# Optimization experiments

Hardware: AMD Instinct MI355X
Metric: run time of the kernel (lower is better)

The kernel has to match this reference:

```python
import jax, jax.numpy as jnp
import numpy as np

NUM_ENVS = 16384
N = 12          # decision vars (4 legs x 3D force)
M_CON = 24      # 4 SOC cones (3 each) + 12-dim hardtanh box
A_MIN, A_MAX = -10.0, 10.0
ALPHA, BETA = 1.0, 1.0


def setup_inputs() -> dict:
    key = jax.random.key(0)
    k1, k2, k3, k4 = jax.random.split(key, 4)
    Mw = jax.random.normal(k1, (NUM_ENVS, N, N), dtype=jnp.float32) / np.sqrt(N)
    # P must be SPD for inv/solve as in the original QP setup
    P = Mw @ jnp.swapaxes(Mw, -1, -2) + jnp.eye(N, dtype=jnp.float32)
    q = jax.random.normal(k2, (NUM_ENVS, N), dtype=jnp.float32)
    H = jax.random.normal(k3, (NUM_ENVS, M_CON, N), dtype=jnp.float32) * 0.5
    b = jax.random.normal(k4, (NUM_ENVS, M_CON), dtype=jnp.float32)
    contact_filter = jnp.ones((NUM_ENVS, M_CON), dtype=jnp.float32)
    return {"P": P, "q": q, "H": H, "b": b, "contact_filter": contact_filter, "iters": 100}


def _project(z, cf):
    # z: [B, m, 1]. Faithful to torch: project_onto_soc's only in-place effect on z
    # is z_part *= (z_part[:, 2:3] > 0); the full cone projection result is
    # discarded (returned but never written back). Then hardtanh box, then contact filter.
    Bsz = z.shape[0]
    soc = z[:, :12].reshape(Bsz, 4, 3)               # 4 cones of dim 3
    soc = soc * (soc[:, :, 2:3] > 0)                 # zero cone block if z-component <= 0
    box = jnp.clip(z[:, 12:24], A_MIN, A_MAX)        # hardtanh
    z = jnp.concatenate([soc.reshape(Bsz, 12, 1), box], axis=1)
    return z * cf


def reference(P, q, H, b, contact_filter, iters):
    m = H.shape[1]
    q_ = q[..., None]                                # [B, n, 1]
    b_ = b[..., None]                                # [B, m, 1]
    cf = contact_filter[..., None]                   # [B, m, 1]
    Ht = jnp.swapaxes(H, -1, -2)
    I = jnp.eye(m, dtype=P.dtype)
    Fm = I - H @ jnp.linalg.inv(P + Ht @ H) @ Ht     # [B, m, m]
    mu = Fm @ (H @ jnp.linalg.solve(P, q_) - b_)     # [B, m, 1]
    A = jnp.concatenate([
        jnp.concatenate([Fm, BETA * Fm], axis=2),
        jnp.concatenate([ALPHA * (I - 2.0 * Fm), I - 2.0 * ALPHA * BETA * Fm], axis=2),
    ], axis=1)                                       # [B, 2m, 2m]
    Bv = jnp.concatenate([BETA * mu, -2.0 * ALPHA * BETA * mu], axis=1)  # [B, 2m, 1]

    def step(lz, _):
        lz = A @ lz + Bv
        lz = jnp.concatenate([lz[:, :m], _project(lz[:, m:], cf)], axis=1)
        return lz, None

    lz0 = jnp.zeros((P.shape[0], 2 * m, 1), dtype=P.dtype)
    lz, _ = jax.lax.scan(step, lz0, None, length=iters)
    x = jnp.linalg.pinv(H) @ (lz[:, m:] - b_)        # [B, n, 1]
    return x, lz
```

## Files before the change

### kernel.cpp

```cpp
#include <hip/hip_runtime.h>

#define EPB 32
#define BLOCK 128
#define HS 292
#define GS 148
#define SS 28

#define WFENCE() __builtin_amdgcn_wave_barrier()

#define DPP_XOR1 0xB1
#define DPP_XOR2 0x4E
#define DPP_QP3  0x1B

typedef float f2 __attribute__((ext_vector_type(2)));

__device__ __forceinline__ f2 pkfma(f2 a, f2 b, f2 c) {
  return __builtin_elementwise_fma(a, b, c);
}

#define FMA4(acc, f, s)                                         \
  acc = fmaf((f).x, (s).x,                                      \
        fmaf((f).y, (s).y,                                      \
        fmaf((f).z, (s).z,                                      \
        fmaf((f).w, (s).w, (acc)))))

#define VFMA(acc, s, v)                                         \
  { (acc).x = fmaf((s), (v).x, (acc).x);                        \
    (acc).y = fmaf((s), (v).y, (acc).y);                        \
    (acc).z = fmaf((s), (v).z, (acc).z);                        \
    (acc).w = fmaf((s), (v).w, (acc).w); }

#define ADD4(A, B) { (A).x += (B).x; (A).y += (B).y; (A).z += (B).z; (A).w += (B).w; }

template<int CTRL>
__device__ __forceinline__ float dppv(float v) {
  return __int_as_float(__builtin_amdgcn_update_dpp(
      0, __float_as_int(v), CTRL, 0xF, 0xF, true));
}

template<int K>
__device__ __forceinline__ float getel(const float4& a, const float4& b, const float4& c) {
  if constexpr (K == 0) return a.x; else if constexpr (K == 1) return a.y;
  else if constexpr (K == 2) return a.z; else if constexpr (K == 3) return a.w;
  else if constexpr (K == 4) return b.x; else if constexpr (K == 5) return b.y;
  else if constexpr (K == 6) return b.z; else if constexpr (K == 7) return b.w;
  else if constexpr (K == 8) return c.x; else if constexpr (K == 9) return c.y;
  else if constexpr (K == 10) return c.z; else return c.w;
}
template<int K>
__device__ __forceinline__ void setel(float4& a, float4& b, float4& c, float v) {
  if constexpr (K == 0) a.x = v; else if constexpr (K == 1) a.y = v;
  else if constexpr (K == 2) a.z = v; else if constexpr (K == 3) a.w = v;
  else if constexpr (K == 4) b.x = v; else if constexpr (K == 5) b.y = v;
  else if constexpr (K == 6) b.z = v; else if constexpr (K == 7) b.w = v;
  else if constexpr (K == 8) c.x = v; else if constexpr (K == 9) c.y = v;
  else if constexpr (K == 10) c.z = v; else c.w = v;
}

__device__ __forceinline__ float dot12(float4 a0, float4 a1, float4 a2,
                                       const float* p) {
  const float4* p4 = (const float4*)p;
  float4 b0 = p4[0], b1 = p4[1], b2 = p4[2];
  float acc = 0.f;
  FMA4(acc, a0, b0); FMA4(acc, a1, b1); FMA4(acc, a2, b2);
  return acc;
}

template<int K>
__device__ __forceinline__ void pivot_pub(float4& a, float4& b, float4& c, float* piv) {
  float ip = 1.0f / getel<K>(a, b, c);
  setel<K>(a, b, c, 1.0f);
  a.x *= ip; a.y *= ip; a.z *= ip; a.w *= ip;
  b.x *= ip; b.y *= ip; b.z *= ip; b.w *= ip;
  c.x *= ip; c.y *= ip; c.z *= ip; c.w *= ip;
  float4* pv = (float4*)piv;
  pv[0] = a; pv[1] = b; pv[2] = c;
}

#define ELIM(f, A, B, C)                                              \
  { (A).x = fmaf(-(f), p0.x, (A).x); (A).y = fmaf(-(f), p0.y, (A).y); \
    (A).z = fmaf(-(f), p0.z, (A).z); (A).w = fmaf(-(f), p0.w, (A).w); \
    (B).x = fmaf(-(f), p1.x, (B).x); (B).y = fmaf(-(f), p1.y, (B).y); \
    (B).z = fmaf(-(f), p1.z, (B).z); (B).w = fmaf(-(f), p1.w, (B).w); \
    (C).x = fmaf(-(f), p2.x, (C).x); (C).y = fmaf(-(f), p2.y, (C).y); \
    (C).z = fmaf(-(f), p2.z, (C).z); (C).w = fmaf(-(f), p2.w, (C).w); }

template<int K>
__device__ __forceinline__ void rgj3_step(
    float4& a0, float4& b0, float4& c0,
    float4& a1, float4& b1, float4& c1,
    float4& a2, float4& b2, float4& c2,
    float* piv, int t) {
  constexpr int SET = K >> 2, OWN = K & 3;
  if (t == OWN) {
    if constexpr (SET == 0)      pivot_pub<K>(a0, b0, c0, piv);
    else if constexpr (SET == 1) pivot_pub<K>(a1, b1, c1, piv);
    else                         pivot_pub<K>(a2, b2, c2, piv);
  }
  WFENCE();
  const float4* pv = (const float4*)piv;
  float4 p0 = pv[0], p1 = pv[1], p2 = pv[2];
  {
    const bool own = (SET == 0) && (t == OWN);
    float cur = getel<K>(a0, b0, c0);
    float f = own ? 0.0f : cur;
    setel<K>(a0, b0, c0, own ? cur : 0.0f);
    ELIM(f, a0, b0, c0);
  }
  {
    const bool own = (SET == 1) && (t == OWN);
    float cur = getel<K>(a1, b1, c1);
    float f = own ? 0.0f : cur;
    setel<K>(a1, b1, c1, own ? cur : 0.0f);
    ELIM(f, a1, b1, c1);
  }
  {
    const bool own = (SET == 2) && (t == OWN);
    float cur = getel<K>(a2, b2, c2);
    float f = own ? 0.0f : cur;
    setel<K>(a2, b2, c2, own ? cur : 0.0f);
    ELIM(f, a2, b2, c2);
  }
  WFENCE();
}

template<int K>
__device__ __forceinline__ void rgj3_all(
    float4& a0, float4& b0, float4& c0,
    float4& a1, float4& b1, float4& c1,
    float4& a2, float4& b2, float4& c2,
    float* piv, int t) {
  rgj3_step<K>(a0, b0, c0, a1, b1, c1, a2, b2, c2, piv, t);
  if constexpr (K < 11) rgj3_all<K + 1>(a0, b0, c0, a1, b1, c1, a2, b2, c2, piv, t);
}

__device__ __forceinline__ void gram3(const float* myH, int t,
    float4& a0, float4& b0, float4& c0,
    float4& a1, float4& b1, float4& c1,
    float4& a2, float4& b2, float4& c2) {
  a0 = make_float4(0.f, 0.f, 0.f, 0.f);
  b0 = a0; c0 = a0; a1 = a0; b1 = a0; c1 = a0; a2 = a0; b2 = a0; c2 = a0;
#pragma unroll
  for (int k = 0; k < 24; ++k) {
    const float4* hk = (const float4*)(myH + k * 12);
    float4 h0 = hk[0], h1 = hk[1], h2 = hk[2];
    float f0 = myH[k * 12 + t];
    float f1 = myH[k * 12 + t + 4];
    float f2v = myH[k * 12 + t + 8];
    VFMA(a0, f0, h0);  VFMA(b0, f0, h1);  VFMA(c0, f0, h2);
    VFMA(a1, f1, h0);  VFMA(b1, f1, h1);  VFMA(c1, f1, h2);
    VFMA(a2, f2v, h0); VFMA(b2, f2v, h1); VFMA(c2, f2v, h2);
  }
}

__device__ __forceinline__ void buildW(const float* myH, const float* gi, int r0,
                                       float4* Wa, float4* Wb, float4* Wc) {
  Wa[0] = make_float4(0.f, 0.f, 0.f, 0.f); Wa[1] = Wa[0]; Wa[2] = Wa[0];
  Wb[0] = Wa[0]; Wb[1] = Wa[0]; Wb[2] = Wa[0];
  Wc[0] = Wa[0]; Wc[1] = Wa[0]; Wc[2] = Wa[0];
#pragma unroll
  for (int c = 0; c < 12; ++c) {
    const float4* g4 = (const float4*)(gi + c * 12);
    float4 r0v = g4[0], r1v = g4[1], r2v = g4[2];
    float k0 = myH[(r0 + 0) * 12 + c];
    float k1 = myH[(r0 + 1) * 12 + c];
    float k2 = myH[(r0 + 2) * 12 + c];
    VFMA(Wa[0], k0, r0v); VFMA(Wa[1], k0, r1v); VFMA(Wa[2], k0, r2v);
    VFMA(Wb[0], k1, r0v); VFMA(Wb[1], k1, r1v); VFMA(Wb[2], k1, r2v);
    VFMA(Wc[0], k2, r0v); VFMA(Wc[1], k2, r1v); VFMA(Wc[2], k2, r2v);
  }
}

template<int m, int k, int base>
__device__ __forceinline__ void slot4(const float* myH, int t,
    const float4* Wa, const float4* Wb, const float4* Wc,
    f2* pA, f2* pB, f2* pC) {
  const int c = 6 * (t ^ m) + k;
  const float4* hc = (const float4*)(myH + c * 12);
  float4 h0 = hc[0], h1 = hc[1], h2 = hc[2];
  float d0 = 0.f, d1 = 0.f, d2 = 0.f;
  FMA4(d0, h0, Wa[0]); FMA4(d0, h1, Wa[1]); FMA4(d0, h2, Wa[2]);
  FMA4(d1, h0, Wb[0]); FMA4(d1, h1, Wb[1]); FMA4(d1, h2, Wb[2]);
  FMA4(d2, h0, Wc[0]); FMA4(d2, h1, Wc[1]); FMA4(d2, h2, Wc[2]);
  float v0 = ((m == 0 && k == base + 0) ? 1.0f : 0.0f) - d0;
  float v1 = ((m == 0 && k == base + 1) ? 1.0f : 0.0f) - d1;
  float v2 = ((m == 0 && k == base + 2) ? 1.0f : 0.0f) - d2;
  constexpr int P = 3 * m + (k >> 1);
  if constexpr ((k & 1) == 0) { pA[P].x = v0; pB[P].x = v1; pC[P].x = v2; }
  else                        { pA[P].y = v0; pB[P].y = v1; pC[P].y = v2; }
}

#define SLOTS(base, pA, pB, pC)                                   \
  slot4<0,0,base>(myH,t,Wa,Wb,Wc,pA,pB,pC);                       \
  slot4<0,1,base>(myH,t,Wa,Wb,Wc,pA,pB,pC);                       \
  slot4<0,2,base>(myH,t,Wa,Wb,Wc,pA,pB,pC);                       \
  slot4<0,3,base>(myH,t,Wa,Wb,Wc,pA,pB,pC);                       \
  slot4<0,4,base>(myH,t,Wa,Wb,Wc,pA,pB,pC);                       \
  slot4<0,5,base>(myH,t,Wa,Wb,Wc,pA,pB,pC);                       \
  slot4<1,0,base>(myH,t,Wa,Wb,Wc,pA,pB,pC);                       \
  slot4<1,1,base>(myH,t,Wa,Wb,Wc,pA,pB,pC);                       \
  slot4<1,2,base>(myH,t,Wa,Wb,Wc,pA,pB,pC);                       \
  slot4<1,3,base>(myH,t,Wa,Wb,Wc,pA,pB,pC);                       \
  slot4<1,4,base>(myH,t,Wa,Wb,Wc,pA,pB,pC);                       \
  slot4<1,5,base>(myH,t,Wa,Wb,Wc,pA,pB,pC);                       \
  slot4<2,0,base>(myH,t,Wa,Wb,Wc,pA,pB,pC);                       \
  slot4<2,1,base>(myH,t,Wa,Wb,Wc,pA,pB,pC);                       \
  slot4<2,2,base>(myH,t,Wa,Wb,Wc,pA,pB,pC);                       \
  slot4<2,3,base>(myH,t,Wa,Wb,Wc,pA,pB,pC);                       \
  slot4<2,4,base>(myH,t,Wa,Wb,Wc,pA,pB,pC);                       \
  slot4<2,5,base>(myH,t,Wa,Wb,Wc,pA,pB,pC);                       \
  slot4<3,0,base>(myH,t,Wa,Wb,Wc,pA,pB,pC);                       \
  slot4<3,1,base>(myH,t,Wa,Wb,Wc,pA,pB,pC);                       \
  slot4<3,2,base>(myH,t,Wa,Wb,Wc,pA,pB,pC);                       \
  slot4<3,3,base>(myH,t,Wa,Wb,Wc,pA,pB,pC);                       \
  slot4<3,4,base>(myH,t,Wa,Wb,Wc,pA,pB,pC);                       \
  slot4<3,5,base>(myH,t,Wa,Wb,Wc,pA,pB,pC);

__global__ __attribute__((amdgpu_flat_work_group_size(BLOCK, BLOCK),
                          amdgpu_waves_per_eu(1, 4)))
void pdhg_kernel(const float* __restrict__ P, const float* __restrict__ q,
                 const float* __restrict__ H, const float* __restrict__ b,
                 const float* __restrict__ cf, const int* __restrict__ itp,
                 float* __restrict__ out, int Btot) {
  __shared__ __align__(16) float sH[EPB * HS];
  __shared__ __align__(16) float sGi[EPB * GS];
  __shared__ __align__(16) float sB[EPB * SS];
  __shared__ __align__(16) float sAux[EPB * SS];

  const int tid  = threadIdx.x;
  const int wq   = tid >> 6;
  const int lane = tid & 63;
  const int g16  = lane >> 2;
  const int t    = lane & 3;
  const int e    = wq * 16 + g16;
  const int env  = blockIdx.x * EPB + e;
  const int envW0 = blockIdx.x * EPB + wq * 16;
  const int niter = itp[0];
  const int r6 = 6 * t;

  {
    const float4* gH = (const float4*)(H + (size_t)envW0 * 288);
#pragma unroll
    for (int rep = 0; rep < 18; ++rep) {
      int i = lane + rep * 64;
      int ee = i / 72, off = i - ee * 72;
      *(float4*)&sH[(wq * 16 + ee) * HS + off * 4] = gH[i];
    }
    const float4* gP = (const float4*)(P + (size_t)envW0 * 144);
#pragma unroll
    for (int rep = 0; rep < 9; ++rep) {
      int i = lane + rep * 64;
      int ee = i / 36, off = i - ee * 36;
      *(float4*)&sGi[(wq * 16 + ee) * GS + off * 4] = gP[i];
    }
    const float4* gq = (const float4*)(q + (size_t)envW0 * 12);
    if (lane < 48) {
      int ee = lane / 3, off = lane - ee * 3;
      *(float4*)&sAux[(wq * 16 + ee) * SS + off * 4] = gq[lane];
    }
    const float4* gb = (const float4*)(b + (size_t)envW0 * 24);
    {
      int i = lane;
      int ee = i / 6, off = i - ee * 6;
      *(float4*)&sB[(wq * 16 + ee) * SS + off * 4] = gb[i];
      if (lane < 32) {
        i = lane + 64;
        ee = i / 6; off = i - ee * 6;
        *(float4*)&sB[(wq * 16 + ee) * SS + off * 4] = gb[i];
      }
    }
  }
  WFENCE();

  const float* myH = &sH[e * HS];
  float* giB  = &sGi[e * GS];
  float* auxB = &sAux[e * SS];
  float* bBm  = &sB[e * SS];
  const float* bB = bBm;

  float4 a0, b0, c0, a1, b1, c1, a2, b2, c2;
  gram3(myH, t, a0, b0, c0, a1, b1, c1, a2, b2, c2);
  {
    const float4* p0 = (const float4*)(giB + t * 12);
    const float4* p1 = (const float4*)(giB + (t + 4) * 12);
    const float4* p2 = (const float4*)(giB + (t + 8) * 12);
    float4 q0 = p0[0], q1 = p0[1], q2 = p0[2];
    float4 r0 = p1[0], r1 = p1[1], r2 = p1[2];
    float4 s0 = p2[0], s1 = p2[1], s2 = p2[2];
    ADD4(a0, q0); ADD4(b0, q1); ADD4(c0, q2);
    ADD4(a1, r0); ADD4(b1, r1); ADD4(c1, r2);
    ADD4(a2, s0); ADD4(b2, s1); ADD4(c2, s2);
  }
  rgj3_all<0>(a0, b0, c0, a1, b1, c1, a2, b2, c2, auxB + 12, t);

  {
    float4* w0 = (float4*)(giB + t * 12);        w0[0] = a0; w0[1] = b0; w0[2] = c0;
    float4* w1 = (float4*)(giB + (t + 4) * 12);  w1[0] = a1; w1[1] = b1; w1[2] = c1;
    float4* w2 = (float4*)(giB + (t + 8) * 12);  w2[0] = a2; w2[1] = b2; w2[2] = c2;
  }
  float y0 = dot12(a0, b0, c0, auxB);
  float y1 = dot12(a1, b1, c1, auxB);
  float y2 = dot12(a2, b2, c2, auxB);
  WFENCE();
  auxB[12 + t] = y0; auxB[16 + t] = y1; auxB[20 + t] = y2;
  WFENCE();

  f2 pm0_[12], pm1_[12], pm2_[12], pm3_[12], pm4_[12], pm5_[12];
  {
    float4 Wa[3], Wb[3], Wc[3];
    buildW(myH, giB, r6 + 0, Wa, Wb, Wc);
    SLOTS(0, pm0_, pm1_, pm2_)
    buildW(myH, giB, r6 + 3, Wa, Wb, Wc);
    SLOTS(3, pm3_, pm4_, pm5_)
  }

  float u0, u1, u2, u3, u4, u5;
  {
    const float4* y4 = (const float4*)(auxB + 12);
    float4 ya = y4[0], yb = y4[1], yc = y4[2];
#define UROW(rr, dst) { const float4* hp = (const float4*)(myH + (r6 + (rr)) * 12); \
      float4 h0 = hp[0], h1 = hp[1], h2 = hp[2]; dst = 0.f;                         \
      FMA4(dst, h0, ya); FMA4(dst, h1, yb); FMA4(dst, h2, yc); }
    UROW(0, u0) UROW(1, u1) UROW(2, u2) UROW(3, u3) UROW(4, u4) UROW(5, u5)
#undef UROW
  }

  float mu0, mu1, mu2, mu3, mu4, mu5;
  {
    const int cA = 6 * (t ^ 1), cB = 6 * (t ^ 2), cC = 6 * (t ^ 3);
    f2 bq0 = { bB[r6 + 0], bB[r6 + 1] };
    f2 bq1 = { bB[r6 + 2], bB[r6 + 3] };
    f2 bq2 = { bB[r6 + 4], bB[r6 + 5] };
    f2 bq3 = { bB[cA + 0], bB[cA + 1] };
    f2 bq4 = { bB[cA + 2], bB[cA + 3] };
    f2 bq5 = { bB[cA + 4], bB[cA + 5] };
    f2 bq6 = { bB[cB + 0], bB[cB + 1] };
    f2 bq7 = { bB[cB + 2], bB[cB + 3] };
    f2 bq8 = { bB[cB + 4], bB[cB + 5] };
    f2 bq9 = { bB[cC + 0], bB[cC + 1] };
    f2 bq10 = { bB[cC + 2], bB[cC + 3] };
    f2 bq11 = { bB[cC + 4], bB[cC + 5] };
#define MUROW(rr, uu) {                                              \
    f2 S1 = {0.f, 0.f}, S2 = {0.f, 0.f};                             \
    S1 = pkfma(pm##rr##_[0], bq0, S1);                               \
    S1 = pkfma(pm##rr##_[1], bq1, S1);                               \
    S1 = pkfma(pm##rr##_[2], bq2, S1);                               \
    S1 = pkfma(pm##rr##_[3], bq3, S1);                               \
    S1 = pkfma(pm##rr##_[4], bq4, S1);                               \
    S1 = pkfma(pm##rr##_[5], bq5, S1);                               \
    S2 = pkfma(pm##rr##_[6], bq6, S2);                               \
    S2 = pkfma(pm##rr##_[7], bq7, S2);                               \
    S2 = pkfma(pm##rr##_[8], bq8, S2);                               \
    S2 = pkfma(pm##rr##_[9], bq9, S2);                               \
    S2 = pkfma(pm##rr##_[10], bq10, S2);                             \
    S2 = pkfma(pm##rr##_[11], bq11, S2);                             \
    f2 St = S1 + S2;                                                 \
    mu##rr = (uu) - (St.x + St.y); }
    MUROW(0, u0) MUROW(1, u1) MUROW(2, u2)
    MUROW(3, u3) MUROW(4, u4) MUROW(5, u5)
#undef MUROW
  }
  const float* cfp = cf + (size_t)env * 24 + r6;
  float cfv0 = cfp[0], cfv1 = cfp[1], cfv2 = cfp[2];
  float cfv3 = cfp[3], cfv4 = cfp[4], cfv5 = cfp[5];

  const float plo  = (t < 2) ? -3.0e38f : -10.0f;
  const float phi  = (t < 2) ?  3.0e38f :  10.0f;
  const float pthr = (t < 2) ? 0.0f     : -3.0e38f;
  float l0 = 0.f, l1 = 0.f, l2 = 0.f, l3 = 0.f, l4 = 0.f, l5 = 0.f;
  float z0 = 0.f, z1 = 0.f, z2 = 0.f, z3 = 0.f, z4 = 0.f, z5 = 0.f;
#pragma unroll 1
  for (int it = 0; it < niter; ++it) {
    f2 q0, q1, q2;
    q0.x = l0 + z0; q0.y = l1 + z1;
    q1.x = l2 + z2; q1.y = l3 + z3;
    q2.x = l4 + z4; q2.y = l5 + z5;
    f2 q3, q4, q5, q6, q7, q8, q9, q10, q11;
    q3.x = dppv<DPP_XOR1>(q0.x);  q3.y = dppv<DPP_XOR1>(q0.y);
    q4.x = dppv<DPP_XOR1>(q1.x);  q4.y = dppv<DPP_XOR1>(q1.y);
    q5.x = dppv<DPP_XOR1>(q2.x);  q5.y = dppv<DPP_XOR1>(q2.y);
    q6.x = dppv<DPP_XOR2>(q0.x);  q6.y = dppv<DPP_XOR2>(q0.y);
    q7.x = dppv<DPP_XOR2>(q1.x);  q7.y = dppv<DPP_XOR2>(q1.y);
    q8.x = dppv<DPP_XOR2>(q2.x);  q8.y = dppv<DPP_XOR2>(q2.y);
    q9.x = dppv<DPP_QP3>(q0.x);   q9.y = dppv<DPP_QP3>(q0.y);
    q10.x = dppv<DPP_QP3>(q1.x);  q10.y = dppv<DPP_QP3>(q1.y);
    q11.x = dppv<DPP_QP3>(q2.x);  q11.y = dppv<DPP_QP3>(q2.y);
#define FMAROW(rr, wdst) {                                           \
    f2 A = { mu##rr, 0.f };                                          \
    f2 Bv = { 0.f, 0.f };                                            \
    A = pkfma(pm##rr##_[0], q0, A);                                  \
    A = pkfma(pm##rr##_[1], q1, A);                                  \
    A = pkfma(pm##rr##_[2], q2, A);                                  \
    A = pkfma(pm##rr##_[3], q3, A);                                  \
    A = pkfma(pm##rr##_[4], q4, A);                                  \
    A = pkfma(pm##rr##_[5], q5, A);                                  \
    Bv = pkfma(pm##rr##_[6], q6, Bv);                                \
    Bv = pkfma(pm##rr##_[7], q7, Bv);                                \
    Bv = pkfma(pm##rr##_[8], q8, Bv);                                \
    Bv = pkfma(pm##rr##_[9], q9, Bv);                                \
    Bv = pkfma(pm##rr##_[10], q10, Bv);                              \
    Bv = pkfma(pm##rr##_[11], q11, Bv);                              \
    f2 C = A + Bv;                                                   \
    wdst = C.x + C.y; }
    float w0, w1, w2, w3, w4, w5;
    FMAROW(0, w0) FMAROW(1, w1) FMAROW(2, w2)
    FMAROW(3, w3) FMAROW(4, w4) FMAROW(5, w5)
#undef FMAROW
    float zp0 = fmaf(-2.0f, w0, q0.x);
    float zp1 = fmaf(-2.0f, w1, q0.y);
    float zp2 = fmaf(-2.0f, w2, q1.x);
    float zp3 = fmaf(-2.0f, w3, q1.y);
    float zp4 = fmaf(-2.0f, w4, q2.x);
    float zp5 = fmaf(-2.0f, w5, q2.y);
    l0 = w0; l1 = w1; l2 = w2; l3 = w3; l4 = w4; l5 = w5;
    bool gA = zp2 > pthr;
    bool gB = zp5 > pthr;
    float e0 = gA ? cfv0 : 0.0f;
    float e1 = gA ? cfv1 : 0.0f;
    float e2 = gA ? cfv2 : 0.0f;
    float e3 = gB ? cfv3 : 0.0f;
    float e4 = gB ? cfv4 : 0.0f;
    float e5 = gB ? cfv5 : 0.0f;
    z0 = __builtin_amdgcn_fmed3f(zp0, plo, phi) * e0;
    z1 = __builtin_amdgcn_fmed3f(zp1, plo, phi) * e1;
    z2 = __builtin_amdgcn_fmed3f(zp2, plo, phi) * e2;
    z3 = __builtin_amdgcn_fmed3f(zp3, plo, phi) * e3;
    z4 = __builtin_amdgcn_fmed3f(zp4, plo, phi) * e4;
    z5 = __builtin_amdgcn_fmed3f(zp5, plo, phi) * e5;
  }

  float* xout  = out;
  float* lzout = out + (size_t)Btot * 12;
  {
    size_t base = (size_t)env * 48 + r6;
    lzout[base + 0] = l0; lzout[base + 1] = l1; lzout[base + 2] = l2;
    lzout[base + 3] = l3; lzout[base + 4] = l4; lzout[base + 5] = l5;
    lzout[base + 24 + 0] = z0; lzout[base + 24 + 1] = z1; lzout[base + 24 + 2] = z2;
    lzout[base + 24 + 3] = z3; lzout[base + 24 + 4] = z4; lzout[base + 24 + 5] = z5;
  }

  float bo0 = bB[r6 + 0], bo1 = bB[r6 + 1], bo2 = bB[r6 + 2];
  float bo3 = bB[r6 + 3], bo4 = bB[r6 + 4], bo5 = bB[r6 + 5];
  WFENCE();
  auxB[r6 + 0] = z0 - bo0; auxB[r6 + 1] = z1 - bo1; auxB[r6 + 2] = z2 - bo2;
  auxB[r6 + 3] = z3 - bo3; auxB[r6 + 4] = z4 - bo4; auxB[r6 + 5] = z5 - bo5;
  WFENCE();

  float rv0 = 0.f, rv1 = 0.f, rv2 = 0.f;
  {
    const float4* a4 = (const float4*)auxB;
    float4 au0 = a4[0], au1 = a4[1], au2 = a4[2], au3 = a4[3], au4 = a4[4], au5 = a4[5];
#define RVS(k, AV) { rv0 = fmaf(myH[(k) * 12 + t],     (AV), rv0);  \
                     rv1 = fmaf(myH[(k) * 12 + t + 4], (AV), rv1);  \
                     rv2 = fmaf(myH[(k) * 12 + t + 8], (AV), rv2); }
    RVS(0,  au0.x) RVS(1,  au0.y) RVS(2,  au0.z) RVS(3,  au0.w)
    RVS(4,  au1.x) RVS(5,  au1.y) RVS(6,  au1.z) RVS(7,  au1.w)
    RVS(8,  au2.x) RVS(9,  au2.y) RVS(10, au2.z) RVS(11, au2.w)
    RVS(12, au3.x) RVS(13, au3.y) RVS(14, au3.z) RVS(15, au3.w)
    RVS(16, au4.x) RVS(17, au4.y) RVS(18, au4.z) RVS(19, au4.w)
    RVS(20, au5.x) RVS(21, au5.y) RVS(22, au5.z) RVS(23, au5.w)
#undef RVS
  }

  gram3(myH, t, a0, b0, c0, a1, b1, c1, a2, b2, c2);
  WFENCE();
  auxB[t] = rv0; auxB[t + 4] = rv1; auxB[t + 8] = rv2;
  WFENCE();
  rgj3_all<0>(a0, b0, c0, a1, b1, c1, a2, b2, c2, bBm, t);

  xout[(size_t)env * 12 + t]     = dot12(a0, b0, c0, auxB);
  xout[(size_t)env * 12 + t + 4] = dot12(a1, b1, c1, auxB);
  xout[(size_t)env * 12 + t + 8] = dot12(a2, b2, c2, auxB);
}

extern "C" void kernel_launch(void* const* d_in, const int* in_sizes, int n_in,
                              void* d_out, int out_size, void* d_ws, size_t ws_size,
                              hipStream_t stream) {
  const float* P  = (const float*)d_in[0];
  const float* q  = (const float*)d_in[1];
  const float* H  = (const float*)d_in[2];
  const float* b  = (const float*)d_in[3];
  const float* cf = (const float*)d_in[4];
  const int*   it = (const int*)d_in[5];
  float* out = (float*)d_out;
  const int B = in_sizes[1] / 12;
  const int grid = B / EPB;
  pdhg_kernel<<<grid, BLOCK, 0, stream>>>(P, q, H, b, cf, it, out, B);
}
```

Before: 130.1 us.

## Broadcast Gauss-Jordan pivot rows via DPP and pack the iteration loop math

The Gauss-Jordan elimination no longer publishes each pivot row through LDS with wave barriers. Every lane now reads the owner lane's row directly through a DPP quad broadcast and computes the reciprocal scaling locally. The iterative loop's projection and update math is also rewritten on packed float2 values, using packed FMA and min/max in place of scalar fmed3. This removes LDS round-trips and fences from the small-matrix inverses and reduces scalar instruction count in the hot loop, at the cost of extra DPP moves per pivot.

Measured after the change: 131.6 us. Within noise of the previous version (+1.1%).

```diff
diff --git a/kernel.cpp b/kernel.cpp
--- a/kernel.cpp
+++ b/kernel.cpp
@@ -66,17 +66,6 @@
   return acc;
 }
 
-template<int K>
-__device__ __forceinline__ void pivot_pub(float4& a, float4& b, float4& c, float* piv) {
-  float ip = 1.0f / getel<K>(a, b, c);
-  setel<K>(a, b, c, 1.0f);
-  a.x *= ip; a.y *= ip; a.z *= ip; a.w *= ip;
-  b.x *= ip; b.y *= ip; b.z *= ip; b.w *= ip;
-  c.x *= ip; c.y *= ip; c.z *= ip; c.w *= ip;
-  float4* pv = (float4*)piv;
-  pv[0] = a; pv[1] = b; pv[2] = c;
-}
-
 #define ELIM(f, A, B, C)                                              \
   { (A).x = fmaf(-(f), p0.x, (A).x); (A).y = fmaf(-(f), p0.y, (A).y); \
     (A).z = fmaf(-(f), p0.z, (A).z); (A).w = fmaf(-(f), p0.w, (A).w); \
@@ -90,16 +79,28 @@
     float4& a0, float4& b0, float4& c0,
     float4& a1, float4& b1, float4& c1,
     float4& a2, float4& b2, float4& c2,
-    float* piv, int t) {
+    int t) {
   constexpr int SET = K >> 2, OWN = K & 3;
+  constexpr int BC = OWN * 0x55;
+  float4 ra, rb, rc;
+  if constexpr (SET == 0)      { ra = a0; rb = b0; rc = c0; }
+  else if constexpr (SET == 1) { ra = a1; rb = b1; rc = c1; }
+  else                         { ra = a2; rb = b2; rc = c2; }
+  float pe = dppv<BC>(getel<K>(ra, rb, rc));
+  float ip = 1.0f / pe;
+  float4 p0, p1, p2;
+  p0.x = dppv<BC>(ra.x) * ip; p0.y = dppv<BC>(ra.y) * ip;
+  p0.z = dppv<BC>(ra.z) * ip; p0.w = dppv<BC>(ra.w) * ip;
+  p1.x = dppv<BC>(rb.x) * ip; p1.y = dppv<BC>(rb.y) * ip;
+  p1.z = dppv<BC>(rb.z) * ip; p1.w = dppv<BC>(rb.w) * ip;
+  p2.x = dppv<BC>(rc.x) * ip; p2.y = dppv<BC>(rc.y) * ip;
+  p2.z = dppv<BC>(rc.z) * ip; p2.w = dppv<BC>(rc.w) * ip;
+  setel<K>(p0, p1, p2, ip);
   if (t == OWN) {
-    if constexpr (SET == 0)      pivot_pub<K>(a0, b0, c0, piv);
-    else if constexpr (SET == 1) pivot_pub<K>(a1, b1, c1, piv);
-    else                         pivot_pub<K>(a2, b2, c2, piv);
-  }
-  WFENCE();
-  const float4* pv = (const float4*)piv;
-  float4 p0 = pv[0], p1 = pv[1], p2 = pv[2];
+    if constexpr (SET == 0)      { a0 = p0; b0 = p1; c0 = p2; }
+    else if constexpr (SET == 1) { a1 = p0; b1 = p1; c1 = p2; }
+    else                         { a2 = p0; b2 = p1; c2 = p2; }
+  }
   {
     const bool own = (SET == 0) && (t == OWN);
     float cur = getel<K>(a0, b0, c0);
@@ -121,7 +122,6 @@
     setel<K>(a2, b2, c2, own ? cur : 0.0f);
     ELIM(f, a2, b2, c2);
   }
-  WFENCE();
 }
 
 template<int K>
@@ -129,9 +129,9 @@
     float4& a0, float4& b0, float4& c0,
     float4& a1, float4& b1, float4& c1,
     float4& a2, float4& b2, float4& c2,
-    float* piv, int t) {
-  rgj3_step<K>(a0, b0, c0, a1, b1, c1, a2, b2, c2, piv, t);
-  if constexpr (K < 11) rgj3_all<K + 1>(a0, b0, c0, a1, b1, c1, a2, b2, c2, piv, t);
+    int t) {
+  rgj3_step<K>(a0, b0, c0, a1, b1, c1, a2, b2, c2, t);
+  if constexpr (K < 11) rgj3_all<K + 1>(a0, b0, c0, a1, b1, c1, a2, b2, c2, t);
 }
 
 __device__ __forceinline__ void gram3(const float* myH, int t,
@@ -291,7 +291,7 @@
     ADD4(a1, r0); ADD4(b1, r1); ADD4(c1, r2);
     ADD4(a2, s0); ADD4(b2, s1); ADD4(c2, s2);
   }
-  rgj3_all<0>(a0, b0, c0, a1, b1, c1, a2, b2, c2, auxB + 12, t);
+  rgj3_all<0>(a0, b0, c0, a1, b1, c1, a2, b2, c2, t);
 
   {
     float4* w0 = (float4*)(giB + t * 12);        w0[0] = a0; w0[1] = b0; w0[2] = c0;
@@ -361,20 +361,23 @@
 #undef MUROW
   }
   const float* cfp = cf + (size_t)env * 24 + r6;
-  float cfv0 = cfp[0], cfv1 = cfp[1], cfv2 = cfp[2];
-  float cfv3 = cfp[3], cfv4 = cfp[4], cfv5 = cfp[5];
+  f2 cf0p = { cfp[0], cfp[1] };
+  f2 cf1p = { cfp[2], cfp[3] };
+  f2 cf2p = { cfp[4], cfp[5] };
 
   const float plo  = (t < 2) ? -3.0e38f : -10.0f;
   const float phi  = (t < 2) ?  3.0e38f :  10.0f;
   const float pthr = (t < 2) ? 0.0f     : -3.0e38f;
-  float l0 = 0.f, l1 = 0.f, l2 = 0.f, l3 = 0.f, l4 = 0.f, l5 = 0.f;
-  float z0 = 0.f, z1 = 0.f, z2 = 0.f, z3 = 0.f, z4 = 0.f, z5 = 0.f;
+  const f2 lo2 = { plo, plo };
+  const f2 hi2 = { phi, phi };
+  const f2 n2  = { -2.0f, -2.0f };
+  f2 l0p = {0.f, 0.f}, l1p = l0p, l2p = l0p;
+  f2 z0p = l0p, z1p = l0p, z2p = l0p;
 #pragma unroll 1
   for (int it = 0; it < niter; ++it) {
-    f2 q0, q1, q2;
-    q0.x = l0 + z0; q0.y = l1 + z1;
-    q1.x = l2 + z2; q1.y = l3 + z3;
-    q2.x = l4 + z4; q2.y = l5 + z5;
+    f2 q0 = l0p + z0p;
+    f2 q1 = l1p + z1p;
+    f2 q2 = l2p + z2p;
     f2 q3, q4, q5, q6, q7, q8, q9, q10, q11;
     q3.x = dppv<DPP_XOR1>(q0.x);  q3.y = dppv<DPP_XOR1>(q0.y);
     q4.x = dppv<DPP_XOR1>(q1.x);  q4.y = dppv<DPP_XOR1>(q1.y);
@@ -402,48 +405,46 @@
     Bv = pkfma(pm##rr##_[11], q11, Bv);                              \
     f2 C = A + Bv;                                                   \
     wdst = C.x + C.y; }
-    float w0, w1, w2, w3, w4, w5;
-    FMAROW(0, w0) FMAROW(1, w1) FMAROW(2, w2)
-    FMAROW(3, w3) FMAROW(4, w4) FMAROW(5, w5)
+    f2 w0p, w1p, w2p;
+    FMAROW(0, w0p.x) FMAROW(1, w0p.y)
+    FMAROW(2, w1p.x) FMAROW(3, w1p.y)
+    FMAROW(4, w2p.x) FMAROW(5, w2p.y)
 #undef FMAROW
-    float zp0 = fmaf(-2.0f, w0, q0.x);
-    float zp1 = fmaf(-2.0f, w1, q0.y);
-    float zp2 = fmaf(-2.0f, w2, q1.x);
-    float zp3 = fmaf(-2.0f, w3, q1.y);
-    float zp4 = fmaf(-2.0f, w4, q2.x);
-    float zp5 = fmaf(-2.0f, w5, q2.y);
-    l0 = w0; l1 = w1; l2 = w2; l3 = w3; l4 = w4; l5 = w5;
-    bool gA = zp2 > pthr;
-    bool gB = zp5 > pthr;
-    float e0 = gA ? cfv0 : 0.0f;
-    float e1 = gA ? cfv1 : 0.0f;
-    float e2 = gA ? cfv2 : 0.0f;
-    float e3 = gB ? cfv3 : 0.0f;
-    float e4 = gB ? cfv4 : 0.0f;
-    float e5 = gB ? cfv5 : 0.0f;
-    z0 = __builtin_amdgcn_fmed3f(zp0, plo, phi) * e0;
-    z1 = __builtin_amdgcn_fmed3f(zp1, plo, phi) * e1;
-    z2 = __builtin_amdgcn_fmed3f(zp2, plo, phi) * e2;
-    z3 = __builtin_amdgcn_fmed3f(zp3, plo, phi) * e3;
-    z4 = __builtin_amdgcn_fmed3f(zp4, plo, phi) * e4;
-    z5 = __builtin_amdgcn_fmed3f(zp5, plo, phi) * e5;
+    f2 zp0 = pkfma(n2, w0p, q0);
+    f2 zp1 = pkfma(n2, w1p, q1);
+    f2 zp2 = pkfma(n2, w2p, q2);
+    l0p = w0p; l1p = w1p; l2p = w2p;
+    bool gA = zp1.x > pthr;
+    bool gB = zp2.y > pthr;
+    f2 c0p = __builtin_elementwise_min(__builtin_elementwise_max(zp0, lo2), hi2);
+    f2 c1p = __builtin_elementwise_min(__builtin_elementwise_max(zp1, lo2), hi2);
+    f2 c2p = __builtin_elementwise_min(__builtin_elementwise_max(zp2, lo2), hi2);
+    f2 m0 = c0p * cf0p;
+    f2 m1 = c1p * cf1p;
+    f2 m2 = c2p * cf2p;
+    z0p.x = gA ? m0.x : 0.0f;
+    z0p.y = gA ? m0.y : 0.0f;
+    z1p.x = gA ? m1.x : 0.0f;
+    z1p.y = gB ? m1.y : 0.0f;
+    z2p.x = gB ? m2.x : 0.0f;
+    z2p.y = gB ? m2.y : 0.0f;
   }
 
   float* xout  = out;
   float* lzout = out + (size_t)Btot * 12;
   {
     size_t base = (size_t)env * 48 + r6;
-    lzout[base + 0] = l0; lzout[base + 1] = l1; lzout[base + 2] = l2;
-    lzout[base + 3] = l3; lzout[base + 4] = l4; lzout[base + 5] = l5;
-    lzout[base + 24 + 0] = z0; lzout[base + 24 + 1] = z1; lzout[base + 24 + 2] = z2;
-    lzout[base + 24 + 3] = z3; lzout[base + 24 + 4] = z4; lzout[base + 24 + 5] = z5;
+    lzout[base + 0] = l0p.x; lzout[base + 1] = l0p.y; lzout[base + 2] = l1p.x;
+    lzout[base + 3] = l1p.y; lzout[base + 4] = l2p.x; lzout[base + 5] = l2p.y;
+    lzout[base + 24 + 0] = z0p.x; lzout[base + 24 + 1] = z0p.y; lzout[base + 24 + 2] = z1p.x;
+    lzout[base + 24 + 3] = z1p.y; lzout[base + 24 + 4] = z2p.x; lzout[base + 24 + 5] = z2p.y;
   }
 
   float bo0 = bB[r6 + 0], bo1 = bB[r6 + 1], bo2 = bB[r6 + 2];
   float bo3 = bB[r6 + 3], bo4 = bB[r6 + 4], bo5 = bB[r6 + 5];
   WFENCE();
-  auxB[r6 + 0] = z0 - bo0; auxB[r6 + 1] = z1 - bo1; auxB[r6 + 2] = z2 - bo2;
-  auxB[r6 + 3] = z3 - bo3; auxB[r6 + 4] = z4 - bo4; auxB[r6 + 5] = z5 - bo5;
+  auxB[r6 + 0] = z0p.x - bo0; auxB[r6 + 1] = z0p.y - bo1; auxB[r6 + 2] = z1p.x - bo2;
+  auxB[r6 + 3] = z1p.y - bo3; auxB[r6 + 4] = z2p.x - bo4; auxB[r6 + 5] = z2p.y - bo5;
   WFENCE();
 
   float rv0 = 0.f, rv1 = 0.f, rv2 = 0.f;
@@ -466,7 +467,7 @@
   WFENCE();
   auxB[t] = rv0; auxB[t + 4] = rv1; auxB[t + 8] = rv2;
   WFENCE();
-  rgj3_all<0>(a0, b0, c0, a1, b1, c1, a2, b2, c2, bBm, t);
+  rgj3_all<0>(a0, b0, c0, a1, b1, c1, a2, b2, c2, t);
 
   xout[(size_t)env * 12 + t]     = dot12(a0, b0, c0, auxB);
   xout[(size_t)env * 12 + t + 4] = dot12(a1, b1, c1, auxB);
```
